# Optimization experiments

Hardware: AMD Instinct MI355X
Metric: run time of the kernel (lower is better)

The kernel has to match this reference:

```python
import jax, jax.numpy as jnp
import numpy as np

B, N, D = 2, 256, 512
H = 4 * D  # mlp_hidden_dim


def setup_inputs() -> dict:
    key = jax.random.key(0)
    ks = jax.random.split(key, 14)
    s_in = 1.0 / np.sqrt(D)
    s_h = 1.0 / np.sqrt(H)
    s_cat = 1.0 / np.sqrt(2 * D)
    return {
        "x_v": jax.random.normal(ks[0], (B, N, D), jnp.float32),
        "x_a": jax.random.normal(ks[1], (B, N, D), jnp.float32),
        # weights stored as (in, out); y = x @ W + b (same math as torch Linear)
        "W1v": jax.random.uniform(ks[2], (D, H), jnp.float32, -s_in, s_in),
        "b1v": jax.random.uniform(ks[3], (H,), jnp.float32, -s_in, s_in),
        "W1a": jax.random.uniform(ks[4], (D, H), jnp.float32, -s_in, s_in),
        "b1a": jax.random.uniform(ks[5], (H,), jnp.float32, -s_in, s_in),
        "Wmv": jax.random.uniform(ks[6], (H, D), jnp.float32, -s_h, s_h),
        "bmv": jax.random.uniform(ks[7], (D,), jnp.float32, -s_h, s_h),
        "Wma": jax.random.uniform(ks[8], (H, D), jnp.float32, -s_h, s_h),
        "bma": jax.random.uniform(ks[9], (D,), jnp.float32, -s_h, s_h),
        "Wout": jax.random.uniform(ks[10], (2 * D, D), jnp.float32, -s_cat, s_cat),
        "bout": jax.random.uniform(ks[11], (D,), jnp.float32, -s_cat, s_cat),
    }


def reference(x_v, x_a, W1v, b1v, W1a, b1a, Wmv, bmv, Wma, bma, Wout, bout):
    # pairwise Manhattan distance: [B, N, M]
    dist = jnp.sum(jnp.abs(x_v[:, :, None, :] - x_a[:, None, :, :]), axis=-1)
    dv = dist.mean(axis=2)  # [B, N] mean distance of each v-token to all a-tokens
    da = dist.mean(axis=1)  # [B, M]
    xv_w = x_v * dv[..., None]
    xa_w = x_a * da[..., None]
    # dropout prob = 0.0 -> identity
    hv = jax.nn.gelu(xv_w @ W1v + b1v, approximate=False) @ Wmv + bmv
    ha = jax.nn.gelu(xa_w @ W1a + b1a, approximate=False) @ Wma + bma
    combined = jnp.concatenate([hv, ha], axis=-1)  # [B, N, 2D]
    return combined @ Wout + bout
```

## Files before the change

### kernel.cpp

```cpp
#include <hip/hip_runtime.h>
#include <math.h>

#define Bsz  2
#define Ntok 256
#define Ddim 512
#define Hdim 2048
#define Mrows 512

typedef __bf16 bf16_8 __attribute__((ext_vector_type(8)));
typedef __bf16 bf16_4 __attribute__((ext_vector_type(4)));
typedef float  f32x4_t __attribute__((ext_vector_type(4)));

struct PrepPtrs {
    const float* src[5];
    __bf16*      dst[5];
    const float* xv;
    const float* xa;
    float*       pv;
    float*       pa;
    float*       out;
};

__global__ __launch_bounds__(256) void prep_kernel(PrepPtrs p) {
    __shared__ float tile[32][33];
    __shared__ float red[4][4];

    int blk = blockIdx.x;
    int tid = threadIdx.x;

    if (blk < 4608) {
        const int Ks[5]  = {512, 512, 2048, 2048, 1024};
        const int Ns[5]  = {2048, 2048, 512, 512, 512};
        const int off[6] = {0, 1024, 2048, 3072, 4096, 4608};
        int mi = 0;
        while (blk >= off[mi + 1]) ++mi;
        int local = blk - off[mi];
        int shift = (mi < 2) ? 6 : 4;
        int bx = local & ((1 << shift) - 1);
        int by = local >> shift;
        const float* src = p.src[mi];
        __bf16*      dst = p.dst[mi];
        int K = Ks[mi], N = Ns[mi];
        int n0 = bx << 5, k0 = by << 5;

        int kl = tid >> 3, nl = (tid & 7) << 2;
        float4 v = *(const float4*)&src[(size_t)(k0 + kl) * N + n0 + nl];
        tile[kl][nl + 0] = v.x;
        tile[kl][nl + 1] = v.y;
        tile[kl][nl + 2] = v.z;
        tile[kl][nl + 3] = v.w;
        __syncthreads();
        int nl2 = tid >> 3, kl2 = (tid & 7) << 2;
        bf16_4 o;
#pragma unroll
        for (int i = 0; i < 4; ++i) o[i] = (__bf16)tile[kl2 + i][nl2];
        *(bf16_4*)&dst[(size_t)(n0 + nl2) * K + k0 + kl2] = o;
    } else if (blk < 5632) {
        int bx   = blk - 4608;
        int jc   = bx & 3;
        int g    = bx >> 2;
        int role = g >> 7;
        int b    = (g >> 6) & 1;
        int i0   = (g & 63) << 2;
        const float* Q    = role ? p.xa : p.xv;
        const float* S    = role ? p.xv : p.xa;
        float*       outp = role ? p.pa : p.pv;

        int d0 = tid << 1;
        const float* Qb = Q + ((size_t)b * Ntok + i0) * Ddim + d0;
        const float* Sb = S + ((size_t)b * Ntok + (jc << 6)) * Ddim + d0;

        float2 q[4];
#pragma unroll
        for (int r = 0; r < 4; ++r) q[r] = *(const float2*)(Qb + r * Ddim);

        float acc[4] = {0.f, 0.f, 0.f, 0.f};
#pragma unroll 4
        for (int j = 0; j < 64; ++j) {
            float2 s = *(const float2*)(Sb + (size_t)j * Ddim);
#pragma unroll
            for (int r = 0; r < 4; ++r)
                acc[r] += fabsf(q[r].x - s.x) + fabsf(q[r].y - s.y);
        }
        int lane = tid & 63, wv = tid >> 6;
#pragma unroll
        for (int r = 0; r < 4; ++r) {
            float v = acc[r];
#pragma unroll
            for (int off2 = 32; off2; off2 >>= 1) v += __shfl_down(v, off2);
            if (lane == 0) red[wv][r] = v;
        }
        __syncthreads();
        if (tid < 4) {
            float v = red[0][tid] + red[1][tid] + red[2][tid] + red[3][tid];
            outp[jc * Mrows + b * Ntok + i0 + tid] = v;
        }
    } else {
        int zb = blk - 5632;
        float4 z4 = {0.f, 0.f, 0.f, 0.f};
        *(float4*)&p.out[((size_t)zb * 256 + tid) * 4] = z4;
    }
}

template <int GELU, int AMODE, int OUTM>
__device__ void gemm_tile(__bf16 (&As)[2][64][40], __bf16 (&Bs)[2][64][40],
                          const void* Aa, const void* Ab, int lda,
                          const __bf16* BT, int ldb,
                          const float* bias, const float* scale4,
                          void* C, int ldc, int Kdim,
                          int m0, int n0, int addBias) {
    const int tid = threadIdx.x;
    const int row = tid >> 2;
    const int kc  = (tid & 3) << 3;

    const __bf16* Bp  = BT + (size_t)(n0 + row) * ldb + kc;
    const float*  Af0 = nullptr;
    const float*  Af1 = nullptr;
    const __bf16* Abp = nullptr;
    float s = 1.0f;
    if (AMODE == 1) {
        Af0 = (const float*)Aa + (size_t)(m0 + row) * lda + kc;
        int m = m0 + row;
        s = (scale4[m] + scale4[Mrows + m] + scale4[2 * Mrows + m] +
             scale4[3 * Mrows + m]) * (1.0f / 256.0f);
    } else if (AMODE == 2) {
        Af0 = (const float*)Aa + (size_t)(m0 + row) * lda + kc;
        Af1 = (const float*)Ab + (size_t)(m0 + row) * lda + kc;
    } else {
        Abp = (const __bf16*)Aa + (size_t)(m0 + row) * lda + kc;
    }

    const int wave = tid >> 6, lane = tid & 63;
    const int moff = (wave >> 1) << 5, noff = (wave & 1) << 5;
    const int lrow = lane & 15, quad = lane >> 4;

    float4 rA0, rA1, rB0, rB1, nA0, nA1, nB0, nB1;
    bf16_8 ra8, na8;
    bf16_8 rb8, nb8;

    auto loadStage = [&](int kt, float4& fa0, float4& fa1, float4& fb0,
                         float4& fb1, bf16_8& a8, bf16_8& b8) {
        b8 = *(const bf16_8*)(Bp + kt);
        if (AMODE == 0) {
            a8 = *(const bf16_8*)(Abp + kt);
        } else {
            fa0 = *(const float4*)(Af0 + kt);
            fa1 = *(const float4*)(Af0 + kt + 4);
            if (AMODE == 2) {
                fb0 = *(const float4*)(Af1 + kt);
                fb1 = *(const float4*)(Af1 + kt + 4);
            }
        }
    };
    auto storeStage = [&](int buf, const float4& fa0, const float4& fa1,
                          const float4& fb0, const float4& fb1,
                          const bf16_8& a8in, const bf16_8& b8in) {
        bf16_8 a8;
        if (AMODE == 0) {
            a8 = a8in;
        } else if (AMODE == 1) {
            a8[0] = (__bf16)(fa0.x * s); a8[1] = (__bf16)(fa0.y * s);
            a8[2] = (__bf16)(fa0.z * s); a8[3] = (__bf16)(fa0.w * s);
            a8[4] = (__bf16)(fa1.x * s); a8[5] = (__bf16)(fa1.y * s);
            a8[6] = (__bf16)(fa1.z * s); a8[7] = (__bf16)(fa1.w * s);
        } else {
            a8[0] = (__bf16)(fa0.x + fb0.x); a8[1] = (__bf16)(fa0.y + fb0.y);
            a8[2] = (__bf16)(fa0.z + fb0.z); a8[3] = (__bf16)(fa0.w + fb0.w);
            a8[4] = (__bf16)(fa1.x + fb1.x); a8[5] = (__bf16)(fa1.y + fb1.y);
            a8[6] = (__bf16)(fa1.z + fb1.z); a8[7] = (__bf16)(fa1.w + fb1.w);
        }
        *(bf16_8*)&As[buf][row][kc] = a8;
        *(bf16_8*)&Bs[buf][row][kc] = b8in;
    };

    f32x4_t acc00 = {0.f, 0.f, 0.f, 0.f};
    f32x4_t acc01 = {0.f, 0.f, 0.f, 0.f};
    f32x4_t acc10 = {0.f, 0.f, 0.f, 0.f};
    f32x4_t acc11 = {0.f, 0.f, 0.f, 0.f};

    const int nIter = Kdim >> 5;

    loadStage(0, rA0, rA1, rB0, rB1, ra8, rb8);
    storeStage(0, rA0, rA1, rB0, rB1, ra8, rb8);
    if (nIter > 1) loadStage(32, rA0, rA1, rB0, rB1, ra8, rb8);
    __syncthreads();

    for (int it = 0; it < nIter; ++it) {
        const int cur = it & 1;
        bf16_8 a0 = *(const bf16_8*)&As[cur][moff + lrow][quad << 3];
        bf16_8 a1 = *(const bf16_8*)&As[cur][moff + 16 + lrow][quad << 3];
        bf16_8 b0 = *(const bf16_8*)&Bs[cur][noff + lrow][quad << 3];
        bf16_8 b1 = *(const bf16_8*)&Bs[cur][noff + 16 + lrow][quad << 3];
        if (it + 2 < nIter)
            loadStage((it + 2) << 5, nA0, nA1, nB0, nB1, na8, nb8);
        acc00 = __builtin_amdgcn_mfma_f32_16x16x32_bf16(a0, b0, acc00, 0, 0, 0);
        acc01 = __builtin_amdgcn_mfma_f32_16x16x32_bf16(a0, b1, acc01, 0, 0, 0);
        acc10 = __builtin_amdgcn_mfma_f32_16x16x32_bf16(a1, b0, acc10, 0, 0, 0);
        acc11 = __builtin_amdgcn_mfma_f32_16x16x32_bf16(a1, b1, acc11, 0, 0, 0);
        if (it + 1 < nIter) {
            storeStage(cur ^ 1, rA0, rA1, rB0, rB1, ra8, rb8);
            rA0 = nA0; rA1 = nA1; rB0 = nB0; rB1 = nB1; ra8 = na8; rb8 = nb8;
            __syncthreads();
        }
    }

    f32x4_t accs[2][2] = {{acc00, acc01}, {acc10, acc11}};
#pragma unroll
    for (int ti = 0; ti < 2; ++ti) {
#pragma unroll
        for (int tj = 0; tj < 2; ++tj) {
            int colg = n0 + noff + (tj << 4) + lrow;
            float bv = addBias ? bias[colg] : 0.0f;
#pragma unroll
            for (int r = 0; r < 4; ++r) {
                int rowg = m0 + moff + (ti << 4) + (quad << 2) + r;
                float v = accs[ti][tj][r] + bv;
                if (GELU) v = 0.5f * v * (1.0f + erff(v * 0.70710678118654752f));
                if (OUTM == 1)
                    ((__bf16*)C)[(size_t)rowg * ldc + colg] = (__bf16)v;
                else if (OUTM == 0)
                    ((float*)C)[(size_t)rowg * ldc + colg] = v;
                else
                    atomicAdd((float*)C + (size_t)rowg * ldc + colg, v);
            }
        }
    }
}

struct FPtrs {
    const float*  x[2];
    const __bf16* WT1[2];
    const float*  b1[2];
    const float*  pd[2];
    __bf16*       g1[2];
    const __bf16* WTm[2];
    const float*  bm[2];
    float*        part[2];
    const __bf16* WTout;
    const float*  bout;
    float*        out;
};

__global__ __launch_bounds__(256) void gemm1_kernel(FPtrs p) {
    __shared__ __align__(16) __bf16 As[2][64][40];
    __shared__ __align__(16) __bf16 Bs[2][64][40];
    int z = blockIdx.z;
    gemm_tile<1, 1, 1>(As, Bs, p.x[z], nullptr, Ddim, p.WT1[z], Ddim,
                       p.b1[z], p.pd[z], p.g1[z], Hdim, Ddim,
                       blockIdx.y << 6, blockIdx.x << 6, 1);
}

__global__ __launch_bounds__(256) void gemm2_kernel(FPtrs p) {
    __shared__ __align__(16) __bf16 As[2][64][40];
    __shared__ __align__(16) __bf16 Bs[2][64][40];
    int zz = blockIdx.z, z = zz & 1, kz = zz >> 1;
    gemm_tile<0, 0, 0>(As, Bs, p.g1[z] + kz * 1024, nullptr, Hdim,
                       p.WTm[z] + kz * 1024, Hdim, p.bm[z], nullptr,
                       p.part[kz] + z * Ddim, 2 * Ddim, 1024,
                       blockIdx.y << 6, blockIdx.x << 6, kz == 0);
}

__global__ __launch_bounds__(256) void gemm3_kernel(FPtrs p) {
    __shared__ __align__(16) __bf16 As[2][64][40];
    __shared__ __align__(16) __bf16 Bs[2][64][40];
    int kz = blockIdx.z;
    gemm_tile<0, 2, 2>(As, Bs, p.part[0] + kz * 256, p.part[1] + kz * 256,
                       2 * Ddim, p.WTout + kz * 256, 2 * Ddim, p.bout,
                       nullptr, p.out, Ddim, 256,
                       blockIdx.y << 6, blockIdx.x << 6, kz == 0);
}

extern "C" void kernel_launch(void* const* d_in, const int* in_sizes, int n_in,
                              void* d_out, int out_size, void* d_ws, size_t ws_size,
                              hipStream_t stream) {
    const float* x_v  = (const float*)d_in[0];
    const float* x_a  = (const float*)d_in[1];
    const float* W1v  = (const float*)d_in[2];
    const float* b1v  = (const float*)d_in[3];
    const float* W1a  = (const float*)d_in[4];
    const float* b1a  = (const float*)d_in[5];
    const float* Wmv  = (const float*)d_in[6];
    const float* bmv  = (const float*)d_in[7];
    const float* Wma  = (const float*)d_in[8];
    const float* bma  = (const float*)d_in[9];
    const float* Wout = (const float*)d_in[10];
    const float* bout = (const float*)d_in[11];
    float* out = (float*)d_out;

    char* w = (char*)d_ws;
    auto alloc = [&](size_t bytes) {
        char* r = w;
        w += (bytes + 255) & ~(size_t)255;
        return (void*)r;
    };
    float*    pv    = (float*)alloc(4 * Mrows * 4);
    float*    pa    = (float*)alloc(4 * Mrows * 4);
    __bf16*   WT1v  = (__bf16*)alloc((size_t)Hdim * Ddim * 2);
    __bf16*   WT1a  = (__bf16*)alloc((size_t)Hdim * Ddim * 2);
    __bf16*   WTmv  = (__bf16*)alloc((size_t)Ddim * Hdim * 2);
    __bf16*   WTma  = (__bf16*)alloc((size_t)Ddim * Hdim * 2);
    __bf16*   WTout = (__bf16*)alloc((size_t)Ddim * 2 * Ddim * 2);
    __bf16*   g1v   = (__bf16*)alloc((size_t)Mrows * Hdim * 2);
    __bf16*   g1a   = (__bf16*)alloc((size_t)Mrows * Hdim * 2);
    float*    part0 = (float*)alloc((size_t)Mrows * 2 * Ddim * 4);
    float*    part1 = (float*)alloc((size_t)Mrows * 2 * Ddim * 4);

    PrepPtrs pp;
    pp.src[0] = W1v;  pp.dst[0] = WT1v;
    pp.src[1] = W1a;  pp.dst[1] = WT1a;
    pp.src[2] = Wmv;  pp.dst[2] = WTmv;
    pp.src[3] = Wma;  pp.dst[3] = WTma;
    pp.src[4] = Wout; pp.dst[4] = WTout;
    pp.xv = x_v; pp.xa = x_a; pp.pv = pv; pp.pa = pa;
    pp.out = out;
    prep_kernel<<<dim3(5888), dim3(256), 0, stream>>>(pp);

    FPtrs fp;
    fp.x[0] = x_v; fp.x[1] = x_a;
    fp.WT1[0] = WT1v; fp.WT1[1] = WT1a;
    fp.b1[0] = b1v; fp.b1[1] = b1a;
    fp.pd[0] = pv; fp.pd[1] = pa;
    fp.g1[0] = g1v; fp.g1[1] = g1a;
    fp.WTm[0] = WTmv; fp.WTm[1] = WTma;
    fp.bm[0] = bmv; fp.bm[1] = bma;
    fp.part[0] = part0; fp.part[1] = part1;
    fp.WTout = WTout; fp.bout = bout;
    fp.out = out;

    gemm1_kernel<<<dim3(Hdim / 64, Mrows / 64, 2), dim3(256), 0, stream>>>(fp);
    gemm2_kernel<<<dim3(8, 8, 4), dim3(256), 0, stream>>>(fp);
    gemm3_kernel<<<dim3(8, 8, 4), dim3(256), 0, stream>>>(fp);
}
```

Baseline: 135.2 us.

## Replace LDS-tiled GEMMs with per-wave register GEMMs and drop split-K atomics

The shared-memory double-buffered block GEMM is replaced by a per-wave GEMM that loads MFMA operands straight from global memory into registers, with 32x32 tiles for gemm1 and 16x16 tiles for gemm2 and gemm3. Split-K partial sums and the atomicAdd output path are removed. gemm2 now writes a bf16 combined buffer and gemm3 does a plain store, so the output zeroing blocks go away. The weight transpose in prep uses 64x64 tiles. In exchange there is no LDS reuse across waves, so global and cache traffic rise, and the intermediate is rounded to bf16.

```diff
diff --git a/kernel.cpp b/kernel.cpp
--- a/kernel.cpp
+++ b/kernel.cpp
@@ -18,45 +18,52 @@
     const float* xa;
     float*       pv;
     float*       pa;
-    float*       out;
 };
 
 __global__ __launch_bounds__(256) void prep_kernel(PrepPtrs p) {
-    __shared__ float tile[32][33];
+    __shared__ float tile[64][65];
     __shared__ float red[4][4];
 
     int blk = blockIdx.x;
     int tid = threadIdx.x;
 
-    if (blk < 4608) {
+    if (blk < 1152) {
         const int Ks[5]  = {512, 512, 2048, 2048, 1024};
         const int Ns[5]  = {2048, 2048, 512, 512, 512};
-        const int off[6] = {0, 1024, 2048, 3072, 4096, 4608};
+        const int off[6] = {0, 256, 512, 768, 1024, 1152};
         int mi = 0;
         while (blk >= off[mi + 1]) ++mi;
         int local = blk - off[mi];
-        int shift = (mi < 2) ? 6 : 4;
+        int shift = (mi < 2) ? 5 : 3;
         int bx = local & ((1 << shift) - 1);
         int by = local >> shift;
         const float* src = p.src[mi];
         __bf16*      dst = p.dst[mi];
         int K = Ks[mi], N = Ns[mi];
-        int n0 = bx << 5, k0 = by << 5;
-
-        int kl = tid >> 3, nl = (tid & 7) << 2;
-        float4 v = *(const float4*)&src[(size_t)(k0 + kl) * N + n0 + nl];
-        tile[kl][nl + 0] = v.x;
-        tile[kl][nl + 1] = v.y;
-        tile[kl][nl + 2] = v.z;
-        tile[kl][nl + 3] = v.w;
+        int n0 = bx << 6, k0 = by << 6;
+
+        int klb = tid >> 4, nl = (tid & 15) << 2;
+#pragma unroll
+        for (int pass = 0; pass < 4; ++pass) {
+            int kl = (pass << 4) + klb;
+            float4 v = *(const float4*)&src[(size_t)(k0 + kl) * N + n0 + nl];
+            tile[kl][nl + 0] = v.x;
+            tile[kl][nl + 1] = v.y;
+            tile[kl][nl + 2] = v.z;
+            tile[kl][nl + 3] = v.w;
+        }
         __syncthreads();
-        int nl2 = tid >> 3, kl2 = (tid & 7) << 2;
-        bf16_4 o;
-#pragma unroll
-        for (int i = 0; i < 4; ++i) o[i] = (__bf16)tile[kl2 + i][nl2];
-        *(bf16_4*)&dst[(size_t)(n0 + nl2) * K + k0 + kl2] = o;
-    } else if (blk < 5632) {
-        int bx   = blk - 4608;
+        int nl2 = tid >> 2, kb = (tid & 3) << 2;
+#pragma unroll
+        for (int pass = 0; pass < 4; ++pass) {
+            int kl2 = (pass << 4) + kb;
+            bf16_4 o;
+#pragma unroll
+            for (int i = 0; i < 4; ++i) o[i] = (__bf16)tile[kl2 + i][nl2];
+            *(bf16_4*)&dst[(size_t)(n0 + nl2) * K + k0 + kl2] = o;
+        }
+    } else {
+        int bx   = blk - 1152;
         int jc   = bx & 3;
         int g    = bx >> 2;
         int role = g >> 7;
@@ -95,133 +102,84 @@
             float v = red[0][tid] + red[1][tid] + red[2][tid] + red[3][tid];
             outp[jc * Mrows + b * Ntok + i0 + tid] = v;
         }
-    } else {
-        int zb = blk - 5632;
-        float4 z4 = {0.f, 0.f, 0.f, 0.f};
-        *(float4*)&p.out[((size_t)zb * 256 + tid) * 4] = z4;
-    }
-}
-
-template <int GELU, int AMODE, int OUTM>
-__device__ void gemm_tile(__bf16 (&As)[2][64][40], __bf16 (&Bs)[2][64][40],
-                          const void* Aa, const void* Ab, int lda,
-                          const __bf16* BT, int ldb,
-                          const float* bias, const float* scale4,
-                          void* C, int ldc, int Kdim,
-                          int m0, int n0, int addBias) {
-    const int tid = threadIdx.x;
-    const int row = tid >> 2;
-    const int kc  = (tid & 3) << 3;
-
-    const __bf16* Bp  = BT + (size_t)(n0 + row) * ldb + kc;
-    const float*  Af0 = nullptr;
-    const float*  Af1 = nullptr;
-    const __bf16* Abp = nullptr;
-    float s = 1.0f;
-    if (AMODE == 1) {
-        Af0 = (const float*)Aa + (size_t)(m0 + row) * lda + kc;
-        int m = m0 + row;
-        s = (scale4[m] + scale4[Mrows + m] + scale4[2 * Mrows + m] +
-             scale4[3 * Mrows + m]) * (1.0f / 256.0f);
-    } else if (AMODE == 2) {
-        Af0 = (const float*)Aa + (size_t)(m0 + row) * lda + kc;
-        Af1 = (const float*)Ab + (size_t)(m0 + row) * lda + kc;
-    } else {
-        Abp = (const __bf16*)Aa + (size_t)(m0 + row) * lda + kc;
-    }
-
-    const int wave = tid >> 6, lane = tid & 63;
-    const int moff = (wave >> 1) << 5, noff = (wave & 1) << 5;
+    }
+}
+
+template <int GELU, int AFP32, int OUTBF16, int MT, int NT>
+__device__ __forceinline__ void wave_gemm(const void* A, int lda,
+                                          const __bf16* BT, int ldb,
+                                          const float* bias, const float* pd,
+                                          void* C, int ldc, int Kdim,
+                                          int m0, int n0) {
+    const int lane = threadIdx.x & 63;
     const int lrow = lane & 15, quad = lane >> 4;
 
-    float4 rA0, rA1, rB0, rB1, nA0, nA1, nB0, nB1;
-    bf16_8 ra8, na8;
-    bf16_8 rb8, nb8;
-
-    auto loadStage = [&](int kt, float4& fa0, float4& fa1, float4& fb0,
-                         float4& fb1, bf16_8& a8, bf16_8& b8) {
-        b8 = *(const bf16_8*)(Bp + kt);
-        if (AMODE == 0) {
-            a8 = *(const bf16_8*)(Abp + kt);
+    const float*  Af[MT];
+    const __bf16* Ab[MT];
+    float s[MT];
+#pragma unroll
+    for (int i = 0; i < MT; ++i) {
+        int row = m0 + (i << 4) + lrow;
+        if (AFP32) {
+            Af[i] = (const float*)A + (size_t)row * lda + (quad << 3);
+            s[i] = (pd[row] + pd[Mrows + row] + pd[2 * Mrows + row] +
+                    pd[3 * Mrows + row]) * (1.0f / 256.0f);
         } else {
-            fa0 = *(const float4*)(Af0 + kt);
-            fa1 = *(const float4*)(Af0 + kt + 4);
-            if (AMODE == 2) {
-                fb0 = *(const float4*)(Af1 + kt);
-                fb1 = *(const float4*)(Af1 + kt + 4);
+            Ab[i] = (const __bf16*)A + (size_t)row * lda + (quad << 3);
+        }
+    }
+    const __bf16* Bp[NT];
+#pragma unroll
+    for (int j = 0; j < NT; ++j)
+        Bp[j] = BT + (size_t)(n0 + (j << 4) + lrow) * ldb + (quad << 3);
+
+    f32x4_t acc[MT][NT];
+#pragma unroll
+    for (int i = 0; i < MT; ++i)
+#pragma unroll
+        for (int j = 0; j < NT; ++j) acc[i][j] = {0.f, 0.f, 0.f, 0.f};
+
+#pragma unroll 4
+    for (int kt = 0; kt < Kdim; kt += 32) {
+        bf16_8 b[NT], a[MT];
+#pragma unroll
+        for (int j = 0; j < NT; ++j) b[j] = *(const bf16_8*)(Bp[j] + kt);
+#pragma unroll
+        for (int i = 0; i < MT; ++i) {
+            if (AFP32) {
+                float4 f0 = *(const float4*)(Af[i] + kt);
+                float4 f1 = *(const float4*)(Af[i] + kt + 4);
+                a[i][0] = (__bf16)(f0.x * s[i]); a[i][1] = (__bf16)(f0.y * s[i]);
+                a[i][2] = (__bf16)(f0.z * s[i]); a[i][3] = (__bf16)(f0.w * s[i]);
+                a[i][4] = (__bf16)(f1.x * s[i]); a[i][5] = (__bf16)(f1.y * s[i]);
+                a[i][6] = (__bf16)(f1.z * s[i]); a[i][7] = (__bf16)(f1.w * s[i]);
+            } else {
+                a[i] = *(const bf16_8*)(Ab[i] + kt);
             }
         }
-    };
-    auto storeStage = [&](int buf, const float4& fa0, const float4& fa1,
-                          const float4& fb0, const float4& fb1,
-                          const bf16_8& a8in, const bf16_8& b8in) {
-        bf16_8 a8;
-        if (AMODE == 0) {
-            a8 = a8in;
-        } else if (AMODE == 1) {
-            a8[0] = (__bf16)(fa0.x * s); a8[1] = (__bf16)(fa0.y * s);
-            a8[2] = (__bf16)(fa0.z * s); a8[3] = (__bf16)(fa0.w * s);
-            a8[4] = (__bf16)(fa1.x * s); a8[5] = (__bf16)(fa1.y * s);
-            a8[6] = (__bf16)(fa1.z * s); a8[7] = (__bf16)(fa1.w * s);
-        } else {
-            a8[0] = (__bf16)(fa0.x + fb0.x); a8[1] = (__bf16)(fa0.y + fb0.y);
-            a8[2] = (__bf16)(fa0.z + fb0.z); a8[3] = (__bf16)(fa0.w + fb0.w);
-            a8[4] = (__bf16)(fa1.x + fb1.x); a8[5] = (__bf16)(fa1.y + fb1.y);
-            a8[6] = (__bf16)(fa1.z + fb1.z); a8[7] = (__bf16)(fa1.w + fb1.w);
-        }
-        *(bf16_8*)&As[buf][row][kc] = a8;
-        *(bf16_8*)&Bs[buf][row][kc] = b8in;
-    };
-
-    f32x4_t acc00 = {0.f, 0.f, 0.f, 0.f};
-    f32x4_t acc01 = {0.f, 0.f, 0.f, 0.f};
-    f32x4_t acc10 = {0.f, 0.f, 0.f, 0.f};
-    f32x4_t acc11 = {0.f, 0.f, 0.f, 0.f};
-
-    const int nIter = Kdim >> 5;
-
-    loadStage(0, rA0, rA1, rB0, rB1, ra8, rb8);
-    storeStage(0, rA0, rA1, rB0, rB1, ra8, rb8);
-    if (nIter > 1) loadStage(32, rA0, rA1, rB0, rB1, ra8, rb8);
-    __syncthreads();
-
-    for (int it = 0; it < nIter; ++it) {
-        const int cur = it & 1;
-        bf16_8 a0 = *(const bf16_8*)&As[cur][moff + lrow][quad << 3];
-        bf16_8 a1 = *(const bf16_8*)&As[cur][moff + 16 + lrow][quad << 3];
-        bf16_8 b0 = *(const bf16_8*)&Bs[cur][noff + lrow][quad << 3];
-        bf16_8 b1 = *(const bf16_8*)&Bs[cur][noff + 16 + lrow][quad << 3];
-        if (it + 2 < nIter)
-            loadStage((it + 2) << 5, nA0, nA1, nB0, nB1, na8, nb8);
-        acc00 = __builtin_amdgcn_mfma_f32_16x16x32_bf16(a0, b0, acc00, 0, 0, 0);
-        acc01 = __builtin_amdgcn_mfma_f32_16x16x32_bf16(a0, b1, acc01, 0, 0, 0);
-        acc10 = __builtin_amdgcn_mfma_f32_16x16x32_bf16(a1, b0, acc10, 0, 0, 0);
-        acc11 = __builtin_amdgcn_mfma_f32_16x16x32_bf16(a1, b1, acc11, 0, 0, 0);
-        if (it + 1 < nIter) {
-            storeStage(cur ^ 1, rA0, rA1, rB0, rB1, ra8, rb8);
-            rA0 = nA0; rA1 = nA1; rB0 = nB0; rB1 = nB1; ra8 = na8; rb8 = nb8;
-            __syncthreads();
-        }
-    }
-
-    f32x4_t accs[2][2] = {{acc00, acc01}, {acc10, acc11}};
-#pragma unroll
-    for (int ti = 0; ti < 2; ++ti) {
-#pragma unroll
-        for (int tj = 0; tj < 2; ++tj) {
-            int colg = n0 + noff + (tj << 4) + lrow;
-            float bv = addBias ? bias[colg] : 0.0f;
+#pragma unroll
+        for (int i = 0; i < MT; ++i)
+#pragma unroll
+            for (int j = 0; j < NT; ++j)
+                acc[i][j] = __builtin_amdgcn_mfma_f32_16x16x32_bf16(
+                    a[i], b[j], acc[i][j], 0, 0, 0);
+    }
+
+#pragma unroll
+    for (int j = 0; j < NT; ++j) {
+        int col = n0 + (j << 4) + lrow;
+        float bv = bias[col];
+#pragma unroll
+        for (int i = 0; i < MT; ++i) {
 #pragma unroll
             for (int r = 0; r < 4; ++r) {
-                int rowg = m0 + moff + (ti << 4) + (quad << 2) + r;
-                float v = accs[ti][tj][r] + bv;
+                int row = m0 + (i << 4) + (quad << 2) + r;
+                float v = acc[i][j][r] + bv;
                 if (GELU) v = 0.5f * v * (1.0f + erff(v * 0.70710678118654752f));
-                if (OUTM == 1)
-                    ((__bf16*)C)[(size_t)rowg * ldc + colg] = (__bf16)v;
-                else if (OUTM == 0)
-                    ((float*)C)[(size_t)rowg * ldc + colg] = v;
+                if (OUTBF16)
+                    ((__bf16*)C)[(size_t)row * ldc + col] = (__bf16)v;
                 else
-                    atomicAdd((float*)C + (size_t)rowg * ldc + colg, v);
+                    ((float*)C)[(size_t)row * ldc + col] = v;
             }
         }
     }
@@ -235,39 +193,35 @@
     __bf16*       g1[2];
     const __bf16* WTm[2];
     const float*  bm[2];
-    float*        part[2];
+    __bf16*       comb;
     const __bf16* WTout;
     const float*  bout;
     float*        out;
 };
 
 __global__ __launch_bounds__(256) void gemm1_kernel(FPtrs p) {
-    __shared__ __align__(16) __bf16 As[2][64][40];
-    __shared__ __align__(16) __bf16 Bs[2][64][40];
-    int z = blockIdx.z;
-    gemm_tile<1, 1, 1>(As, Bs, p.x[z], nullptr, Ddim, p.WT1[z], Ddim,
-                       p.b1[z], p.pd[z], p.g1[z], Hdim, Ddim,
-                       blockIdx.y << 6, blockIdx.x << 6, 1);
+    int gw = (blockIdx.x << 2) + (threadIdx.x >> 6);
+    int z = gw >> 10, t = gw & 1023;
+    int mt = t >> 6, nt = t & 63;
+    wave_gemm<1, 1, 1, 2, 2>(p.x[z], Ddim, p.WT1[z], Ddim, p.b1[z], p.pd[z],
+                             p.g1[z], Hdim, Ddim, mt << 5, nt << 5);
 }
 
 __global__ __launch_bounds__(256) void gemm2_kernel(FPtrs p) {
-    __shared__ __align__(16) __bf16 As[2][64][40];
-    __shared__ __align__(16) __bf16 Bs[2][64][40];
-    int zz = blockIdx.z, z = zz & 1, kz = zz >> 1;
-    gemm_tile<0, 0, 0>(As, Bs, p.g1[z] + kz * 1024, nullptr, Hdim,
-                       p.WTm[z] + kz * 1024, Hdim, p.bm[z], nullptr,
-                       p.part[kz] + z * Ddim, 2 * Ddim, 1024,
-                       blockIdx.y << 6, blockIdx.x << 6, kz == 0);
+    int gw = (blockIdx.x << 2) + (threadIdx.x >> 6);
+    int z = gw >> 10, t = gw & 1023;
+    int mt = t >> 5, nt = t & 31;
+    wave_gemm<0, 0, 1, 1, 1>(p.g1[z], Hdim, p.WTm[z], Hdim, p.bm[z], nullptr,
+                             p.comb + (size_t)z * Ddim, 2 * Ddim, Hdim,
+                             mt << 4, nt << 4);
 }
 
 __global__ __launch_bounds__(256) void gemm3_kernel(FPtrs p) {
-    __shared__ __align__(16) __bf16 As[2][64][40];
-    __shared__ __align__(16) __bf16 Bs[2][64][40];
-    int kz = blockIdx.z;
-    gemm_tile<0, 2, 2>(As, Bs, p.part[0] + kz * 256, p.part[1] + kz * 256,
-                       2 * Ddim, p.WTout + kz * 256, 2 * Ddim, p.bout,
-                       nullptr, p.out, Ddim, 256,
-                       blockIdx.y << 6, blockIdx.x << 6, kz == 0);
+    int gw = (blockIdx.x << 2) + (threadIdx.x >> 6);
+    int mt = gw >> 5, nt = gw & 31;
+    wave_gemm<0, 0, 0, 1, 1>(p.comb, 2 * Ddim, p.WTout, 2 * Ddim, p.bout,
+                             nullptr, p.out, Ddim, 2 * Ddim,
+                             mt << 4, nt << 4);
 }
 
 extern "C" void kernel_launch(void* const* d_in, const int* in_sizes, int n_in,
@@ -302,8 +256,7 @@
     __bf16*   WTout = (__bf16*)alloc((size_t)Ddim * 2 * Ddim * 2);
     __bf16*   g1v   = (__bf16*)alloc((size_t)Mrows * Hdim * 2);
     __bf16*   g1a   = (__bf16*)alloc((size_t)Mrows * Hdim * 2);
-    float*    part0 = (float*)alloc((size_t)Mrows * 2 * Ddim * 4);
-    float*    part1 = (float*)alloc((size_t)Mrows * 2 * Ddim * 4);
+    __bf16*   comb  = (__bf16*)alloc((size_t)Mrows * 2 * Ddim * 2);
 
     PrepPtrs pp;
     pp.src[0] = W1v;  pp.dst[0] = WT1v;
@@ -312,8 +265,7 @@
     pp.src[3] = Wma;  pp.dst[3] = WTma;
     pp.src[4] = Wout; pp.dst[4] = WTout;
     pp.xv = x_v; pp.xa = x_a; pp.pv = pv; pp.pa = pa;
-    pp.out = out;
-    prep_kernel<<<dim3(5888), dim3(256), 0, stream>>>(pp);
+    prep_kernel<<<dim3(2176), dim3(256), 0, stream>>>(pp);
 
     FPtrs fp;
     fp.x[0] = x_v; fp.x[1] = x_a;
@@ -323,11 +275,11 @@
     fp.g1[0] = g1v; fp.g1[1] = g1a;
     fp.WTm[0] = WTmv; fp.WTm[1] = WTma;
     fp.bm[0] = bmv; fp.bm[1] = bma;
-    fp.part[0] = part0; fp.part[1] = part1;
+    fp.comb = comb;
     fp.WTout = WTout; fp.bout = bout;
     fp.out = out;
 
-    gemm1_kernel<<<dim3(Hdim / 64, Mrows / 64, 2), dim3(256), 0, stream>>>(fp);
-    gemm2_kernel<<<dim3(8, 8, 4), dim3(256), 0, stream>>>(fp);
-    gemm3_kernel<<<dim3(8, 8, 4), dim3(256), 0, stream>>>(fp);
-}
+    gemm1_kernel<<<dim3(512), dim3(256), 0, stream>>>(fp);
+    gemm2_kernel<<<dim3(512), dim3(256), 0, stream>>>(fp);
+    gemm3_kernel<<<dim3(256), dim3(256), 0, stream>>>(fp);
+}
```

Result: slower. 167.9 us (+24.2%).
